# Performance work log

Measured on AMD Instinct MI355X. Metric: run time of the kernel, lower is better.

Reference implementation:

```python
import jax, jax.numpy as jnp
from jax import lax
import numpy as np


def setup_inputs() -> dict:
    key = jax.random.key(0)
    ks = jax.random.split(key, 5)
    B = 256
    data = jax.random.normal(ks[0], (B, 1, 28, 28), jnp.float32)
    # ConvLayer: Conv2d(1->256, k=9, s=1)
    w1 = jax.random.normal(ks[1], (256, 1, 9, 9), jnp.float32) * 0.1
    b1 = jnp.zeros((256,), jnp.float32)
    # PrimaryCaps: Conv2d(256->256, k=9, s=2)
    w2 = jax.random.normal(ks[2], (256, 256, 9, 9), jnp.float32) * 0.02
    b2 = jnp.zeros((256,), jnp.float32)
    # DigitCaps routing weights: (in_caps=1152, out_caps=10, out_len=16, in_len=8)
    W = jax.random.normal(ks[3], (1152, 10, 16, 8), jnp.float32) * 0.05
    return {"data": data, "w1": w1, "b1": b1, "w2": w2, "b2": b2, "W": W}


def _squash(s):
    # s: (B,1,10,16); sn*s / ((1+sn)*sqrt(sn)) as in the torch code
    sn = jnp.sum(s * s, axis=-1, keepdims=True)
    return sn * s / ((1.0 + sn) * jnp.sqrt(sn))


def reference(data, w1, b1, w2, b2, W):
    # ConvLayer: conv k9 s1 VALID + relu -> (B,256,20,20)
    x = lax.conv(data, w1, (1, 1), 'VALID') + b1[None, :, None, None]
    x = jax.nn.relu(x)
    # PrimaryCaps: conv k9 s2 VALID -> (B,256,6,6)
    x = lax.conv(x, w2, (2, 2), 'VALID') + b2[None, :, None, None]
    B = x.shape[0]
    # toCapsules: (B,256,6,6) -> (B,8,32,6,6) -> (B,8,1152) -> (B,1152,8)
    x = x.reshape(B, 8, -1).transpose(0, 2, 1)
    # u_hat[b,n,o,k] = W[n,o,k,d] @ x[b,n,d]  -> (B,1152,10,16)
    u_hat = jnp.einsum('nokd,bnd->bnok', W, x)
    b_ij = jnp.zeros((B, 1152, 10, 1), u_hat.dtype)
    num_iterations = 3
    v_j = None
    for it in range(1, num_iterations + 1):
        c_ij = jax.nn.softmax(b_ij, axis=1)            # over input capsules
        s_j = jnp.sum(c_ij * u_hat, axis=1, keepdims=True)  # (B,1,10,16)
        v_j = _squash(s_j)
        if it < num_iterations:
            # Faithful to the torch code: a_ij = u_hat * sum_k(v_j), broadcast
            # over input capsules; b_ij widens to (B,1152,10,16) after iter 1.
            a_ij = u_hat * jnp.sum(v_j, axis=-1, keepdims=True)
            b_ij = b_ij + a_ij
    return v_j[:, 0]  # (B,10,16)
```

## Files before the change

kernel.cpp:

```cpp
#include <hip/hip_runtime.h>
#include <hip/hip_bf16.h>
#include <cmath>


typedef float f32x4 __attribute__((ext_vector_type(4)));
typedef short s16x8 __attribute__((ext_vector_type(8)));
typedef unsigned int u32;

static __device__ __forceinline__ short f2bf(float x) {
  __hip_bfloat16 h = __float2bfloat16(x);
  return *reinterpret_cast<short*>(&h);
}
static __device__ __forceinline__ float bf2f(short s) {
  __hip_bfloat16 h;
  *reinterpret_cast<short*>(&h) = s;
  return __bfloat162float(h);
}
static __device__ __forceinline__ void stage16(const short* g, short* l) {
  __builtin_amdgcn_global_load_lds(
      (const __attribute__((address_space(1))) u32*)(const void*)g,
      (__attribute__((address_space(3))) u32*)(void*)l, 16, 0, 0);
}

#define CHUNK_SHORTS 23552
#define ODD_OFS 12288
#define EV_IMG 12288
#define OD_IMG 11264

__global__ __launch_bounds__(256) void prep_all(
    const float* __restrict__ w2, s16x8* __restrict__ wstg,
    const float* __restrict__ data, const float* __restrict__ w1,
    const float* __restrict__ b1, short* __restrict__ c1g) {
  __shared__ float sbuf[12784];
  const int t = threadIdx.x;
  if (blockIdx.x < 512) {
    const int b = blockIdx.x;
    const int chunk = b >> 6;
    const int kg = (b >> 4) & 3;
    const int cot = b & 15;
    const int co0 = cot * 16;
    const size_t gbase = (size_t)(chunk * 32 + kg * 8) * 81;
    for (int i = t; i < 10368; i += 256) {
      const int r = i / 648, e = i - r * 648;
      sbuf[i] = w2[(size_t)(co0 + r) * 20736 + gbase + e];
    }
    __syncthreads();
    for (int p = t; p < 1296; p += 256) {
      const int tap = p >> 4, co = p & 15;
      s16x8 hi, lo;
#pragma unroll
      for (int i = 0; i < 8; ++i) {
        const float x = sbuf[co * 648 + i * 81 + tap];
        const short h = f2bf(x);
        hi[i] = h;
        lo[i] = f2bf(x - bf2f(h));
      }
      const size_t T = (size_t)(chunk * 81 + tap);
      wstg[T * 2048 + kg * 256 + co0 + co] = hi;
      wstg[T * 2048 + 1024 + kg * 256 + co0 + co] = lo;
    }
    return;
  }
  const int cb = blockIdx.x - 512;
  const int img = cb >> 1;
  const int chh = cb & 1;
  float* simg = sbuf;
  short* c1buf = (short*)&sbuf[1008];
  for (int i = t; i < 784; i += 256)
    simg[(i / 28) * 36 + (i % 28)] = data[img * 784 + i];
  __syncthreads();
  for (int cc = 0; cc < 4; ++cc) {
    const int chunk = chh * 4 + cc;
    for (int task = t; task < 608; task += 256) {
      const int ci = task & 31;
      const int y = task >> 5;
      const int ch = chunk * 32 + ci;
      const float* wr = w1 + ch * 81;
      float acc[20];
      const float bz = b1[ch];
#pragma unroll
      for (int x = 0; x < 20; ++x) acc[x] = bz;
#pragma unroll
      for (int ky = 0; ky < 9; ++ky) {
        float rr[28];
#pragma unroll
        for (int q = 0; q < 7; ++q)
          *(float4*)&rr[q * 4] = *(const float4*)&simg[(y + ky) * 36 + q * 4];
#pragma unroll
        for (int kx = 0; kx < 9; ++kx) {
          const float w = wr[ky * 9 + kx];
#pragma unroll
          for (int x = 0; x < 20; ++x) acc[x] = fmaf(w, rr[x + kx], acc[x]);
        }
      }
      const int kg = ci >> 3, il = ci & 7;
#pragma unroll
      for (int x = 0; x < 19; ++x) {
        const int xh = x >> 1;
        const int r = (x & 1) ? (y * 9 + xh) : (y * 10 + xh);
        short* base = c1buf + ((x & 1) ? ODD_OFS : 0);
        const float v = fmaxf(acc[x], 0.f);
        const short hi = f2bf(v);
        const short lo = f2bf(v - bf2f(hi));
        base[r * 64 + (((kg + r) & 7) << 3) + il] = hi;
        base[r * 64 + (((kg + 4 + r) & 7) << 3) + il] = lo;
      }
    }
    __syncthreads();
    {
      s16x8* dst = (s16x8*)(c1g + (size_t)(img * 8 + chunk) * CHUNK_SHORTS);
      const s16x8* srcb = (const s16x8*)c1buf;
      for (int i = t; i < 2944; i += 256) dst[i] = srcb[i];
    }
    __syncthreads();
  }
}

__global__ __launch_bounds__(256) void conv2_mfma(
    const short* __restrict__ c1g, const short* __restrict__ wstg,
    const float* __restrict__ b2, float* __restrict__ xcaps0,
    float* __restrict__ xcaps1) {
  const int t = threadIdx.x;
  const int bid = blockIdx.x;
  const int xcd = bid & 7;
  const int ksp = xcd & 1;
  const int coh = (xcd >> 1) & 1;
  const int pair = (bid >> 3) * 2 + (xcd >> 2);
  const int img0 = pair * 2;
  const int lane = t & 63;
  const int wv = t >> 6;
  const int r16 = lane & 15;
  const int kg = lane >> 4;

  __shared__ short c1[24576];

  int arowE[5], arowO[5], imE[5], imO[5];
#pragma unroll
  for (int m = 0; m < 5; ++m) {
    const int s = m * 16 + r16;
    const int im = (s >= 36) ? 1 : 0;
    int p = s - 36 * im;
    if (p > 35) p = 35;
    const int oy = p / 6, ox = p % 6;
    arowE[m] = oy * 20 + ox;
    arowO[m] = oy * 18 + ox;
    imE[m] = im * EV_IMG;
    imO[m] = im * OD_IMG;
  }
  int bOff[2], con[2];
  float bias[2];
#pragma unroll
  for (int j = 0; j < 2; ++j) {
    const int co = coh * 128 + wv * 32 + j * 16 + r16;
    con[j] = co;
    bOff[j] = kg * 256 + co;
    bias[j] = (ksp == 0) ? b2[co] : 0.f;
  }
  float* xcp = (ksp == 0) ? xcaps0 : xcaps1;

  const f32x4 vzero = {0.f, 0.f, 0.f, 0.f};
  f32x4 acc[5][2];
#pragma unroll
  for (int m = 0; m < 5; ++m)
#pragma unroll
    for (int j = 0; j < 2; ++j) acc[m][j] = vzero;

  const s16x8* wsv = (const s16x8*)wstg;

  for (int cc = 0; cc < 4; ++cc) {
    const int chunk = ksp * 4 + cc;
    const short* src0 = c1g + (size_t)(img0 * 8 + chunk) * CHUNK_SHORTS;
    const short* src1 = c1g + (size_t)((img0 + 1) * 8 + chunk) * CHUNK_SHORTS;
    const size_t bb = (size_t)chunk * 81 * 2048;

    __syncthreads();
    for (int c = wv; c < 48; c += 4) {
      const short* s = (c < 24) ? (src0 + c * 512) : (src1 + (c - 24) * 512);
      stage16(s + lane * 8, &c1[c * 512]);
    }
    __syncthreads();
    {
      s16x8 BHc[2], BLc[2];
#pragma unroll
      for (int j = 0; j < 2; ++j) {
        BHc[j] = wsv[bb + bOff[j]];
        BLc[j] = wsv[bb + bOff[j] + 1024];
      }
      for (int ky = 0; ky < 9; ++ky) {
#pragma unroll
        for (int kxi = 0; kxi < 5; ++kxi) {
          s16x8 BHn[2], BLn[2];
          if (!(ky == 8 && kxi == 4)) {
            const int nky = (kxi == 4) ? ky + 1 : ky;
            const int nkxi = (kxi == 4) ? 0 : kxi + 1;
            const size_t nb = bb + (size_t)(nky * 9 + 2 * nkxi) * 2048;
#pragma unroll
            for (int j = 0; j < 2; ++j) {
              BHn[j] = wsv[nb + bOff[j]];
              BLn[j] = wsv[nb + bOff[j] + 1024];
            }
          }
          s16x8 AH[5], AL[5];
#pragma unroll
          for (int m = 0; m < 5; ++m) {
            const int r = arowE[m] + ky * 10 + kxi;
            AH[m] = *(const s16x8*)&c1[imE[m] + r * 64 + (((kg + r) & 7) << 3)];
            AL[m] = *(const s16x8*)&c1[imE[m] + r * 64 + (((kg + 4 + r) & 7) << 3)];
          }
          __builtin_amdgcn_s_setprio(1);
#pragma unroll
          for (int m = 0; m < 5; ++m)
#pragma unroll
            for (int j = 0; j < 2; ++j)
              acc[m][j] = __builtin_amdgcn_mfma_f32_16x16x32_bf16(AH[m], BHc[j], acc[m][j], 0, 0, 0);
#pragma unroll
          for (int m = 0; m < 5; ++m)
#pragma unroll
            for (int j = 0; j < 2; ++j)
              acc[m][j] = __builtin_amdgcn_mfma_f32_16x16x32_bf16(AL[m], BHc[j], acc[m][j], 0, 0, 0);
#pragma unroll
          for (int m = 0; m < 5; ++m)
#pragma unroll
            for (int j = 0; j < 2; ++j)
              acc[m][j] = __builtin_amdgcn_mfma_f32_16x16x32_bf16(AH[m], BLc[j], acc[m][j], 0, 0, 0);
          __builtin_amdgcn_s_setprio(0);
#pragma unroll
          for (int j = 0; j < 2; ++j) { BHc[j] = BHn[j]; BLc[j] = BLn[j]; }
        }
      }
    }

    __syncthreads();
    for (int c = wv; c < 44; c += 4) {
      const short* s = (c < 22) ? (src0 + ODD_OFS + c * 512)
                                : (src1 + ODD_OFS + (c - 22) * 512);
      stage16(s + lane * 8, &c1[c * 512]);
    }
    __syncthreads();
    {
      s16x8 BHc[2], BLc[2];
#pragma unroll
      for (int j = 0; j < 2; ++j) {
        BHc[j] = wsv[bb + 2048 + bOff[j]];
        BLc[j] = wsv[bb + 2048 + bOff[j] + 1024];
      }
      for (int ky = 0; ky < 9; ++ky) {
#pragma unroll
        for (int kxi = 0; kxi < 4; ++kxi) {
          s16x8 BHn[2], BLn[2];
          if (!(ky == 8 && kxi == 3)) {
            const int nky = (kxi == 3) ? ky + 1 : ky;
            const int nkxi = (kxi == 3) ? 0 : kxi + 1;
            const size_t nb = bb + (size_t)(nky * 9 + 2 * nkxi + 1) * 2048;
#pragma unroll
            for (int j = 0; j < 2; ++j) {
              BHn[j] = wsv[nb + bOff[j]];
              BLn[j] = wsv[nb + bOff[j] + 1024];
            }
          }
          s16x8 AH[5], AL[5];
#pragma unroll
          for (int m = 0; m < 5; ++m) {
            const int r = arowO[m] + ky * 9 + kxi;
            AH[m] = *(const s16x8*)&c1[imO[m] + r * 64 + (((kg + r) & 7) << 3)];
            AL[m] = *(const s16x8*)&c1[imO[m] + r * 64 + (((kg + 4 + r) & 7) << 3)];
          }
          __builtin_amdgcn_s_setprio(1);
#pragma unroll
          for (int m = 0; m < 5; ++m)
#pragma unroll
            for (int j = 0; j < 2; ++j)
              acc[m][j] = __builtin_amdgcn_mfma_f32_16x16x32_bf16(AH[m], BHc[j], acc[m][j], 0, 0, 0);
#pragma unroll
          for (int m = 0; m < 5; ++m)
#pragma unroll
            for (int j = 0; j < 2; ++j)
              acc[m][j] = __builtin_amdgcn_mfma_f32_16x16x32_bf16(AL[m], BHc[j], acc[m][j], 0, 0, 0);
#pragma unroll
          for (int m = 0; m < 5; ++m)
#pragma unroll
            for (int j = 0; j < 2; ++j)
              acc[m][j] = __builtin_amdgcn_mfma_f32_16x16x32_bf16(AH[m], BLc[j], acc[m][j], 0, 0, 0);
          __builtin_amdgcn_s_setprio(0);
#pragma unroll
          for (int j = 0; j < 2; ++j) { BHc[j] = BHn[j]; BLc[j] = BLn[j]; }
        }
      }
    }
  }

#pragma unroll
  for (int m = 0; m < 5; ++m) {
#pragma unroll
    for (int jj = 0; jj < 4; ++jj) {
      const int s = m * 16 + kg * 4 + jj;
      if (s < 72) {
        const int im = (s >= 36) ? 1 : 0;
        const int p = s - 36 * im;
#pragma unroll
        for (int j = 0; j < 2; ++j) {
          const int co = con[j];
          const int n = (co & 31) * 36 + p;
          xcp[((size_t)(img0 + im) * 1152 + n) * 8 + (co >> 5)] =
              acc[m][j][jj] + bias[j];
        }
      }
    }
  }
}

__global__ __launch_bounds__(256) void routing_fused(const float* __restrict__ xcaps0,
                                                     const float* __restrict__ xcaps1,
                                                     const float* __restrict__ W,
                                                     float* __restrict__ out) {
  const int o = blockIdx.x >> 7;
  const int bp = blockIdx.x & 127;
  const int b0 = bp * 2, b1 = b0 + 1;
  const int t = threadIdx.x;
  const int k = t & 15, ng = t >> 4;
  __shared__ float xs0[1152 * 8];
  __shared__ float xs1[1152 * 8];
  __shared__ double redA[256], redB[256], redC[256], redD[256];
  __shared__ float s0s[16], s1s[16];
  __shared__ float sv0, sv1;
  __shared__ double f0, f1;

  {
    const float4* p00 = (const float4*)(xcaps0 + (size_t)b0 * 9216);
    const float4* p01 = (const float4*)(xcaps1 + (size_t)b0 * 9216);
    const float4* p10 = (const float4*)(xcaps0 + (size_t)b1 * 9216);
    const float4* p11 = (const float4*)(xcaps1 + (size_t)b1 * 9216);
    float4* d0 = (float4*)xs0;
    float4* d1 = (float4*)xs1;
    for (int i = t; i < 2304; i += 256) {
      float4 a = p00[i], b = p01[i];
      float4 c = p10[i], d = p11[i];
      float4 s0, s1;
      s0.x = a.x + b.x; s0.y = a.y + b.y; s0.z = a.z + b.z; s0.w = a.w + b.w;
      s1.x = c.x + d.x; s1.y = c.y + d.y; s1.z = c.z + d.z; s1.w = c.w + d.w;
      d0[i] = s0;
      d1[i] = s1;
    }
  }
  __syncthreads();

  const int n0 = ng * 72;
  float u0[72], u1[72];
  const float* wp = W + ((size_t)(n0 * 10 + o) * 16 + k) * 8;
#pragma unroll
  for (int i = 0; i < 72; ++i) {
    const float* wq = wp + (size_t)i * 1280;
    const float4 wa = *(const float4*)wq;
    const float4 wb = *(const float4*)(wq + 4);
    const float4 xa0 = *(const float4*)&xs0[(n0 + i) * 8];
    const float4 xb0 = *(const float4*)&xs0[(n0 + i) * 8 + 4];
    const float4 xa1 = *(const float4*)&xs1[(n0 + i) * 8];
    const float4 xb1 = *(const float4*)&xs1[(n0 + i) * 8 + 4];
    float s0 = wa.x * xa0.x + wa.y * xa0.y + wa.z * xa0.z + wa.w * xa0.w
             + wb.x * xb0.x + wb.y * xb0.y + wb.z * xb0.z + wb.w * xb0.w;
    float s1 = wa.x * xa1.x + wa.y * xa1.y + wa.z * xa1.z + wa.w * xa1.w
             + wb.x * xb1.x + wb.y * xb1.y + wb.z * xb1.z + wb.w * xb1.w;
    u0[i] = s0;
    u1[i] = s1;
  }

  {
    double S0 = 0.0, S1 = 0.0;
#pragma unroll
    for (int i = 0; i < 72; ++i) { S0 += (double)u0[i]; S1 += (double)u1[i]; }
    redA[t] = S0; redB[t] = S1;
  }
  __syncthreads();
  if (t < 16) {
    double t0 = 0.0, t1 = 0.0;
#pragma unroll
    for (int g = 0; g < 16; ++g) { t0 += redA[g * 16 + t]; t1 += redB[g * 16 + t]; }
    s0s[t] = (float)(t0 * (double)(1.0f / 1152.0f));
    s1s[t] = (float)(t1 * (double)(1.0f / 1152.0f));
  }
  __syncthreads();
  if (t == 0) {
    double sn = 0.0;
#pragma unroll
    for (int kk = 0; kk < 16; ++kk) sn += (double)s0s[kk] * (double)s0s[kk];
    double f = sn / ((1.0 + sn) * sqrt(sn));
    double sv = 0.0;
#pragma unroll
    for (int kk = 0; kk < 16; ++kk) sv += (double)s0s[kk] * f;
    sv0 = (float)sv;
    sn = 0.0;
#pragma unroll
    for (int kk = 0; kk < 16; ++kk) sn += (double)s1s[kk] * (double)s1s[kk];
    f = sn / ((1.0 + sn) * sqrt(sn));
    sv = 0.0;
#pragma unroll
    for (int kk = 0; kk < 16; ++kk) sv += (double)s1s[kk] * f;
    sv1 = (float)sv;
  }
  __syncthreads();
  const float v10 = sv0, v11 = sv1;

  {
    double E0 = 0.0, EU0 = 0.0, E1 = 0.0, EU1 = 0.0;
#pragma unroll
    for (int i = 0; i < 72; ++i) {
      const float e0 = expf(u0[i] * v10);
      E0 += (double)e0;
      EU0 += (double)e0 * (double)u0[i];
      const float e1 = expf(u1[i] * v11);
      E1 += (double)e1;
      EU1 += (double)e1 * (double)u1[i];
    }
    redA[t] = E0; redB[t] = EU0; redC[t] = E1; redD[t] = EU1;
  }
  __syncthreads();
  if (t < 16) {
    double e0 = 0.0, s0 = 0.0, e1 = 0.0, s1 = 0.0;
#pragma unroll
    for (int g = 0; g < 16; ++g) {
      e0 += redA[g * 16 + t]; s0 += redB[g * 16 + t];
      e1 += redC[g * 16 + t]; s1 += redD[g * 16 + t];
    }
    s0s[t] = (float)(s0 / e0);
    s1s[t] = (float)(s1 / e1);
  }
  __syncthreads();
  if (t == 0) {
    double sn = 0.0;
#pragma unroll
    for (int kk = 0; kk < 16; ++kk) sn += (double)s0s[kk] * (double)s0s[kk];
    double f = sn / ((1.0 + sn) * sqrt(sn));
    double sv = 0.0;
#pragma unroll
    for (int kk = 0; kk < 16; ++kk) sv += (double)s0s[kk] * f;
    sv0 = v10 + (float)sv;
    sn = 0.0;
#pragma unroll
    for (int kk = 0; kk < 16; ++kk) sn += (double)s1s[kk] * (double)s1s[kk];
    f = sn / ((1.0 + sn) * sqrt(sn));
    sv = 0.0;
#pragma unroll
    for (int kk = 0; kk < 16; ++kk) sv += (double)s1s[kk] * f;
    sv1 = v11 + (float)sv;
  }
  __syncthreads();
  const float v20 = sv0, v21 = sv1;

  {
    double E0 = 0.0, EU0 = 0.0, E1 = 0.0, EU1 = 0.0;
#pragma unroll
    for (int i = 0; i < 72; ++i) {
      const float e0 = expf(u0[i] * v20);
      E0 += (double)e0;
      EU0 += (double)e0 * (double)u0[i];
      const float e1 = expf(u1[i] * v21);
      E1 += (double)e1;
      EU1 += (double)e1 * (double)u1[i];
    }
    redA[t] = E0; redB[t] = EU0; redC[t] = E1; redD[t] = EU1;
  }
  __syncthreads();
  if (t < 16) {
    double e0 = 0.0, s0 = 0.0, e1 = 0.0, s1 = 0.0;
#pragma unroll
    for (int g = 0; g < 16; ++g) {
      e0 += redA[g * 16 + t]; s0 += redB[g * 16 + t];
      e1 += redC[g * 16 + t]; s1 += redD[g * 16 + t];
    }
    s0s[t] = (float)(s0 / e0);
    s1s[t] = (float)(s1 / e1);
  }
  __syncthreads();
  if (t == 0) {
    double sn = 0.0;
#pragma unroll
    for (int kk = 0; kk < 16; ++kk) sn += (double)s0s[kk] * (double)s0s[kk];
    f0 = sn / ((1.0 + sn) * sqrt(sn));
    sn = 0.0;
#pragma unroll
    for (int kk = 0; kk < 16; ++kk) sn += (double)s1s[kk] * (double)s1s[kk];
    f1 = sn / ((1.0 + sn) * sqrt(sn));
  }
  __syncthreads();
  if (t < 16) {
    out[b0 * 160 + o * 16 + t] = (float)((double)s0s[t] * f0);
    out[b1 * 160 + o * 16 + t] = (float)((double)s1s[t] * f1);
  }
}

extern "C" void kernel_launch(void* const* d_in, const int* in_sizes, int n_in,
                              void* d_out, int out_size, void* d_ws, size_t ws_size,
                              hipStream_t stream) {
  const float* data = (const float*)d_in[0];
  const float* w1   = (const float*)d_in[1];
  const float* b1   = (const float*)d_in[2];
  const float* w2   = (const float*)d_in[3];
  const float* b2   = (const float*)d_in[4];
  const float* W    = (const float*)d_in[5];
  float* out = (float*)d_out;

  short* wstg   = (short*)d_ws;
  short* c1g    = wstg + 10616832;
  float* xcaps0 = (float*)(c1g + 48234496);
  float* xcaps1 = xcaps0 + 2359296;

  prep_all<<<1024, 256, 0, stream>>>(w2, (s16x8*)wstg, data, w1, b1, c1g);
  conv2_mfma<<<512, 256, 0, stream>>>(c1g, wstg, b2, xcaps0, xcaps1);
  routing_fused<<<1280, 256, 0, stream>>>(xcaps0, xcaps1, W, out);
}
```

Baseline: 465.2 us.

## Double routing block threads and use wave shuffles for reductions

The routing kernel now runs 512 threads per block, so each thread holds 36 input capsules instead of 72. That halves the per-thread u_hat register arrays and the serial exp/accumulate work. The LDS tree reductions are replaced by xor-shuffle reductions inside each wave, followed by a small cross-wave sum over 8 partials. The squash steps for the two images now run in parallel on two threads. The intent is to cut register pressure, raise latency hiding, and shorten the serial reduction phases, at the cost of more threads competing for the same LDS-resident capsule data.

```diff
diff --git a/kernel.cpp b/kernel.cpp
--- a/kernel.cpp
+++ b/kernel.cpp
@@ -309,7 +309,7 @@
   }
 }
 
-__global__ __launch_bounds__(256) void routing_fused(const float* __restrict__ xcaps0,
+__global__ __launch_bounds__(512) void routing_fused(const float* __restrict__ xcaps0,
                                                      const float* __restrict__ xcaps1,
                                                      const float* __restrict__ W,
                                                      float* __restrict__ out) {
@@ -318,12 +318,13 @@
   const int b0 = bp * 2, b1 = b0 + 1;
   const int t = threadIdx.x;
   const int k = t & 15, ng = t >> 4;
+  const int lane = t & 63, wavei = t >> 6;
   __shared__ float xs0[1152 * 8];
   __shared__ float xs1[1152 * 8];
-  __shared__ double redA[256], redB[256], redC[256], redD[256];
+  __shared__ double srA[8][16], srB[8][16], srC[8][16], srD[8][16];
   __shared__ float s0s[16], s1s[16];
-  __shared__ float sv0, sv1;
-  __shared__ double f0, f1;
+  __shared__ float sv0s, sv1s;
+  __shared__ double f0s, f1s;
 
   {
     const float4* p00 = (const float4*)(xcaps0 + (size_t)b0 * 9216);
@@ -332,7 +333,7 @@
     const float4* p11 = (const float4*)(xcaps1 + (size_t)b1 * 9216);
     float4* d0 = (float4*)xs0;
     float4* d1 = (float4*)xs1;
-    for (int i = t; i < 2304; i += 256) {
+    for (int i = t; i < 2304; i += 512) {
       float4 a = p00[i], b = p01[i];
       float4 c = p10[i], d = p11[i];
       float4 s0, s1;
@@ -344,11 +345,11 @@
   }
   __syncthreads();
 
-  const int n0 = ng * 72;
-  float u0[72], u1[72];
+  const int n0 = ng * 36;
+  float u0[36], u1[36];
   const float* wp = W + ((size_t)(n0 * 10 + o) * 16 + k) * 8;
 #pragma unroll
-  for (int i = 0; i < 72; ++i) {
+  for (int i = 0; i < 36; ++i) {
     const float* wq = wp + (size_t)i * 1280;
     const float4 wa = *(const float4*)wq;
     const float4 wb = *(const float4*)(wq + 4);
@@ -356,54 +357,48 @@
     const float4 xb0 = *(const float4*)&xs0[(n0 + i) * 8 + 4];
     const float4 xa1 = *(const float4*)&xs1[(n0 + i) * 8];
     const float4 xb1 = *(const float4*)&xs1[(n0 + i) * 8 + 4];
-    float s0 = wa.x * xa0.x + wa.y * xa0.y + wa.z * xa0.z + wa.w * xa0.w
-             + wb.x * xb0.x + wb.y * xb0.y + wb.z * xb0.z + wb.w * xb0.w;
-    float s1 = wa.x * xa1.x + wa.y * xa1.y + wa.z * xa1.z + wa.w * xa1.w
-             + wb.x * xb1.x + wb.y * xb1.y + wb.z * xb1.z + wb.w * xb1.w;
-    u0[i] = s0;
-    u1[i] = s1;
+    u0[i] = wa.x * xa0.x + wa.y * xa0.y + wa.z * xa0.z + wa.w * xa0.w
+          + wb.x * xb0.x + wb.y * xb0.y + wb.z * xb0.z + wb.w * xb0.w;
+    u1[i] = wa.x * xa1.x + wa.y * xa1.y + wa.z * xa1.z + wa.w * xa1.w
+          + wb.x * xb1.x + wb.y * xb1.y + wb.z * xb1.z + wb.w * xb1.w;
   }
 
   {
     double S0 = 0.0, S1 = 0.0;
 #pragma unroll
-    for (int i = 0; i < 72; ++i) { S0 += (double)u0[i]; S1 += (double)u1[i]; }
-    redA[t] = S0; redB[t] = S1;
-  }
-  __syncthreads();
-  if (t < 16) {
-    double t0 = 0.0, t1 = 0.0;
-#pragma unroll
-    for (int g = 0; g < 16; ++g) { t0 += redA[g * 16 + t]; t1 += redB[g * 16 + t]; }
-    s0s[t] = (float)(t0 * (double)(1.0f / 1152.0f));
-    s1s[t] = (float)(t1 * (double)(1.0f / 1152.0f));
-  }
-  __syncthreads();
-  if (t == 0) {
+    for (int i = 0; i < 36; ++i) { S0 += (double)u0[i]; S1 += (double)u1[i]; }
+    S0 += __shfl_xor(S0, 16); S0 += __shfl_xor(S0, 32);
+    S1 += __shfl_xor(S1, 16); S1 += __shfl_xor(S1, 32);
+    if (lane < 16) { srA[wavei][lane] = S0; srB[wavei][lane] = S1; }
+  }
+  __syncthreads();
+  if (t < 32) {
+    const int g = t >> 4, kk = t & 15;
+    double tot = 0.0;
+#pragma unroll
+    for (int w = 0; w < 8; ++w) tot += (g == 0) ? srA[w][kk] : srB[w][kk];
+    if (g == 0) s0s[kk] = (float)(tot * (double)(1.0f / 1152.0f));
+    else        s1s[kk] = (float)(tot * (double)(1.0f / 1152.0f));
+  }
+  __syncthreads();
+  if (t < 2) {
+    const float* ss = (t == 0) ? s0s : s1s;
     double sn = 0.0;
 #pragma unroll
-    for (int kk = 0; kk < 16; ++kk) sn += (double)s0s[kk] * (double)s0s[kk];
-    double f = sn / ((1.0 + sn) * sqrt(sn));
+    for (int kk = 0; kk < 16; ++kk) sn += (double)ss[kk] * (double)ss[kk];
+    const double f = sn / ((1.0 + sn) * sqrt(sn));
     double sv = 0.0;
 #pragma unroll
-    for (int kk = 0; kk < 16; ++kk) sv += (double)s0s[kk] * f;
-    sv0 = (float)sv;
-    sn = 0.0;
-#pragma unroll
-    for (int kk = 0; kk < 16; ++kk) sn += (double)s1s[kk] * (double)s1s[kk];
-    f = sn / ((1.0 + sn) * sqrt(sn));
-    sv = 0.0;
-#pragma unroll
-    for (int kk = 0; kk < 16; ++kk) sv += (double)s1s[kk] * f;
-    sv1 = (float)sv;
-  }
-  __syncthreads();
-  const float v10 = sv0, v11 = sv1;
+    for (int kk = 0; kk < 16; ++kk) sv += (double)ss[kk] * f;
+    if (t == 0) sv0s = (float)sv; else sv1s = (float)sv;
+  }
+  __syncthreads();
+  const float v10 = sv0s, v11 = sv1s;
 
   {
     double E0 = 0.0, EU0 = 0.0, E1 = 0.0, EU1 = 0.0;
 #pragma unroll
-    for (int i = 0; i < 72; ++i) {
+    for (int i = 0; i < 36; ++i) {
       const float e0 = expf(u0[i] * v10);
       E0 += (double)e0;
       EU0 += (double)e0 * (double)u0[i];
@@ -411,45 +406,46 @@
       E1 += (double)e1;
       EU1 += (double)e1 * (double)u1[i];
     }
-    redA[t] = E0; redB[t] = EU0; redC[t] = E1; redD[t] = EU1;
-  }
-  __syncthreads();
-  if (t < 16) {
-    double e0 = 0.0, s0 = 0.0, e1 = 0.0, s1 = 0.0;
-#pragma unroll
-    for (int g = 0; g < 16; ++g) {
-      e0 += redA[g * 16 + t]; s0 += redB[g * 16 + t];
-      e1 += redC[g * 16 + t]; s1 += redD[g * 16 + t];
-    }
-    s0s[t] = (float)(s0 / e0);
-    s1s[t] = (float)(s1 / e1);
-  }
-  __syncthreads();
-  if (t == 0) {
+    E0 += __shfl_xor(E0, 16); E0 += __shfl_xor(E0, 32);
+    EU0 += __shfl_xor(EU0, 16); EU0 += __shfl_xor(EU0, 32);
+    E1 += __shfl_xor(E1, 16); E1 += __shfl_xor(E1, 32);
+    EU1 += __shfl_xor(EU1, 16); EU1 += __shfl_xor(EU1, 32);
+    if (lane < 16) {
+      srA[wavei][lane] = E0; srB[wavei][lane] = EU0;
+      srC[wavei][lane] = E1; srD[wavei][lane] = EU1;
+    }
+  }
+  __syncthreads();
+  if (t < 32) {
+    const int g = t >> 4, kk = t & 15;
+    double te = 0.0, tu = 0.0;
+#pragma unroll
+    for (int w = 0; w < 8; ++w) {
+      te += (g == 0) ? srA[w][kk] : srC[w][kk];
+      tu += (g == 0) ? srB[w][kk] : srD[w][kk];
+    }
+    if (g == 0) s0s[kk] = (float)(tu / te);
+    else        s1s[kk] = (float)(tu / te);
+  }
+  __syncthreads();
+  if (t < 2) {
+    const float* ss = (t == 0) ? s0s : s1s;
     double sn = 0.0;
 #pragma unroll
-    for (int kk = 0; kk < 16; ++kk) sn += (double)s0s[kk] * (double)s0s[kk];
-    double f = sn / ((1.0 + sn) * sqrt(sn));
+    for (int kk = 0; kk < 16; ++kk) sn += (double)ss[kk] * (double)ss[kk];
+    const double f = sn / ((1.0 + sn) * sqrt(sn));
     double sv = 0.0;
 #pragma unroll
-    for (int kk = 0; kk < 16; ++kk) sv += (double)s0s[kk] * f;
-    sv0 = v10 + (float)sv;
-    sn = 0.0;
-#pragma unroll
-    for (int kk = 0; kk < 16; ++kk) sn += (double)s1s[kk] * (double)s1s[kk];
-    f = sn / ((1.0 + sn) * sqrt(sn));
-    sv = 0.0;
-#pragma unroll
-    for (int kk = 0; kk < 16; ++kk) sv += (double)s1s[kk] * f;
-    sv1 = v11 + (float)sv;
-  }
-  __syncthreads();
-  const float v20 = sv0, v21 = sv1;
+    for (int kk = 0; kk < 16; ++kk) sv += (double)ss[kk] * f;
+    if (t == 0) sv0s = v10 + (float)sv; else sv1s = v11 + (float)sv;
+  }
+  __syncthreads();
+  const float v20 = sv0s, v21 = sv1s;
 
   {
     double E0 = 0.0, EU0 = 0.0, E1 = 0.0, EU1 = 0.0;
 #pragma unroll
-    for (int i = 0; i < 72; ++i) {
+    for (int i = 0; i < 36; ++i) {
       const float e0 = expf(u0[i] * v20);
       E0 += (double)e0;
       EU0 += (double)e0 * (double)u0[i];
@@ -457,34 +453,43 @@
       E1 += (double)e1;
       EU1 += (double)e1 * (double)u1[i];
     }
-    redA[t] = E0; redB[t] = EU0; redC[t] = E1; redD[t] = EU1;
-  }
-  __syncthreads();
-  if (t < 16) {
-    double e0 = 0.0, s0 = 0.0, e1 = 0.0, s1 = 0.0;
-#pragma unroll
-    for (int g = 0; g < 16; ++g) {
-      e0 += redA[g * 16 + t]; s0 += redB[g * 16 + t];
-      e1 += redC[g * 16 + t]; s1 += redD[g * 16 + t];
-    }
-    s0s[t] = (float)(s0 / e0);
-    s1s[t] = (float)(s1 / e1);
-  }
-  __syncthreads();
-  if (t == 0) {
+    E0 += __shfl_xor(E0, 16); E0 += __shfl_xor(E0, 32);
+    EU0 += __shfl_xor(EU0, 16); EU0 += __shfl_xor(EU0, 32);
+    E1 += __shfl_xor(E1, 16); E1 += __shfl_xor(E1, 32);
+    EU1 += __shfl_xor(EU1, 16); EU1 += __shfl_xor(EU1, 32);
+    if (lane < 16) {
+      srA[wavei][lane] = E0; srB[wavei][lane] = EU0;
+      srC[wavei][lane] = E1; srD[wavei][lane] = EU1;
+    }
+  }
+  __syncthreads();
+  if (t < 32) {
+    const int g = t >> 4, kk = t & 15;
+    double te = 0.0, tu = 0.0;
+#pragma unroll
+    for (int w = 0; w < 8; ++w) {
+      te += (g == 0) ? srA[w][kk] : srC[w][kk];
+      tu += (g == 0) ? srB[w][kk] : srD[w][kk];
+    }
+    if (g == 0) s0s[kk] = (float)(tu / te);
+    else        s1s[kk] = (float)(tu / te);
+  }
+  __syncthreads();
+  if (t < 2) {
+    const float* ss = (t == 0) ? s0s : s1s;
     double sn = 0.0;
 #pragma unroll
-    for (int kk = 0; kk < 16; ++kk) sn += (double)s0s[kk] * (double)s0s[kk];
-    f0 = sn / ((1.0 + sn) * sqrt(sn));
-    sn = 0.0;
-#pragma unroll
-    for (int kk = 0; kk < 16; ++kk) sn += (double)s1s[kk] * (double)s1s[kk];
-    f1 = sn / ((1.0 + sn) * sqrt(sn));
-  }
-  __syncthreads();
-  if (t < 16) {
-    out[b0 * 160 + o * 16 + t] = (float)((double)s0s[t] * f0);
-    out[b1 * 160 + o * 16 + t] = (float)((double)s1s[t] * f1);
+    for (int kk = 0; kk < 16; ++kk) sn += (double)ss[kk] * (double)ss[kk];
+    if (t == 0) f0s = sn / ((1.0 + sn) * sqrt(sn));
+    else        f1s = sn / ((1.0 + sn) * sqrt(sn));
+  }
+  __syncthreads();
+  if (t < 32) {
+    const int g = t >> 4, kk = t & 15;
+    const int b = (g == 0) ? b0 : b1;
+    const double f = (g == 0) ? f0s : f1s;
+    const float s = (g == 0) ? s0s[kk] : s1s[kk];
+    out[b * 160 + o * 16 + kk] = (float)((double)s * f);
   }
 }
 
@@ -506,5 +511,5 @@
 
   prep_all<<<1024, 256, 0, stream>>>(w2, (s16x8*)wstg, data, w1, b1, c1g);
   conv2_mfma<<<512, 256, 0, stream>>>(c1g, wstg, b2, xcaps0, xcaps1);
-  routing_fused<<<1280, 256, 0, stream>>>(xcaps0, xcaps1, W, out);
-}
+  routing_fused<<<1280, 512, 0, stream>>>(xcaps0, xcaps1, W, out);
+}
```

After: 439.5 us, median of 2. 1.06x faster.
